# Kernel optimization log

Measured on AMD Instinct MI355X. Metric: run time of the kernel, lower is better.

## Reference

```python
import jax, jax.numpy as jnp
import numpy as np

N = 50000
EPS = 1e-5


def gcn_conv(x, edge_index, W, b):
    # x: [N, Fin] -> [N, Fout]; symmetric-normalized aggregation with self-loops
    h = x @ W  # [N, Fout]
    src = jnp.concatenate([edge_index[0], jnp.arange(N, dtype=edge_index.dtype)])
    dst = jnp.concatenate([edge_index[1], jnp.arange(N, dtype=edge_index.dtype)])
    deg = jax.ops.segment_sum(jnp.ones_like(dst, dtype=h.dtype), dst, num_segments=N)
    dinv = jnp.where(deg > 0, jax.lax.rsqrt(deg), 0.0)
    norm = dinv[src] * dinv[dst]  # [E+N]
    msg = h[src] * norm[:, None]  # [E+N, Fout]
    out = jax.ops.segment_sum(msg, dst, num_segments=N)
    return out + b


def batch_norm_eval(x, gamma, beta, mean, var):
    return (x - mean) * jax.lax.rsqrt(var + EPS) * gamma + beta


def setup_inputs() -> dict:
    key = jax.random.key(0)
    ks = jax.random.split(key, 16)
    Fin, H, C = 128, 64, 40
    inp = {
        "x": jax.random.normal(ks[0], (N, Fin), dtype=jnp.float32),
        "edge_index": jax.random.randint(ks[1], (2, 1600000), 0, N, dtype=jnp.int64),
        "W1": jax.random.normal(ks[2], (Fin, H), dtype=jnp.float32) / np.sqrt(Fin),
        "b1": jnp.zeros((H,), jnp.float32),
        "g1": jax.random.normal(ks[3], (H,), jnp.float32) * 0.1 + 1.0,
        "be1": jax.random.normal(ks[4], (H,), jnp.float32) * 0.1,
        "m1": jax.random.normal(ks[5], (H,), jnp.float32) * 0.1,
        "v1": jax.random.uniform(ks[6], (H,), jnp.float32, 0.5, 1.5),
        "W2": jax.random.normal(ks[7], (H, H), dtype=jnp.float32) / np.sqrt(H),
        "b2": jnp.zeros((H,), jnp.float32),
        "g2": jax.random.normal(ks[8], (H,), jnp.float32) * 0.1 + 1.0,
        "be2": jax.random.normal(ks[9], (H,), jnp.float32) * 0.1,
        "m2": jax.random.normal(ks[10], (H,), jnp.float32) * 0.1,
        "v2": jax.random.uniform(ks[11], (H,), jnp.float32, 0.5, 1.5),
        "W3": jax.random.normal(ks[12], (H, C), dtype=jnp.float32) / np.sqrt(H),
        "b3": jnp.zeros((C,), jnp.float32),
    }
    return inp


def reference(x, edge_index, W1, b1, g1, be1, m1, v1, W2, b2, g2, be2, m2, v2, W3, b3):
    # eval-mode forward: dropout is identity, BatchNorm uses running stats
    h = gcn_conv(x, edge_index, W1, b1)
    h = jax.nn.relu(batch_norm_eval(h, g1, be1, m1, v1))
    h = gcn_conv(h, edge_index, W2, b2)
    h = jax.nn.relu(batch_norm_eval(h, g2, be2, m2, v2))
    return gcn_conv(h, edge_index, W3, b3)
```

## Files before the change

kernel.cpp:

```cpp
#include <hip/hip_runtime.h>
#include <hip/hip_fp16.h>

#define BN_EPS 1e-5f

typedef _Float16 half2_t __attribute__((ext_vector_type(2)));
typedef _Float16 half8_t __attribute__((ext_vector_type(8)));

static __device__ __forceinline__ float fdot2(half2_t a, half2_t b, float c) {
    return __builtin_amdgcn_fdot2(a, b, c, false);
}


__global__ void k_zero(int* __restrict__ p, int n) {
    int i = threadIdx.x;
    if (i < n) p[i] = 0;
}

__global__ void k_bcount(const int* __restrict__ dst, int* __restrict__ btot, int E, int B) {
    __shared__ int cnt[256];
    int tid = threadIdx.x;
    cnt[tid] = 0;
    __syncthreads();
    int e0 = blockIdx.x * 2048;
#pragma unroll
    for (int j = 0; j < 8; ++j) {
        int e = e0 + j * 256 + tid;
        if (e < E) atomicAdd(&cnt[dst[e] >> 8], 1);
    }
    __syncthreads();
    if (tid < B && cnt[tid] > 0) atomicAdd(&btot[tid], cnt[tid]);
}

__global__ void k_bscan(const int* __restrict__ btot, int* __restrict__ bbase,
                        int* __restrict__ bcur, int* __restrict__ row_ptr, int N, int B) {
    __shared__ int sc[256];
    int tid = threadIdx.x;
    int v = (tid < B) ? btot[tid] : 0;
    sc[tid] = v;
    __syncthreads();
    for (int off = 1; off < 256; off <<= 1) {
        int t = (tid >= off) ? sc[tid - off] : 0;
        __syncthreads();
        sc[tid] += t;
        __syncthreads();
    }
    int excl = sc[tid] - v;
    if (tid < B) { bbase[tid] = excl; bcur[tid] = excl; }
    if (tid == B - 1) { bbase[B] = excl + v; row_ptr[N] = excl + v; }
}

__global__ void k_bscatter(const int* __restrict__ src, const int* __restrict__ dst,
                           int* bcur, unsigned int* __restrict__ ebuf, int E, int B) {
    __shared__ int cnt[256];
    __shared__ int gb[256];
    int tid = threadIdx.x;
    cnt[tid] = 0;
    __syncthreads();
    int e0 = blockIdx.x * 2048;
    int bk[8], rk[8];
    unsigned int pay[8];
#pragma unroll
    for (int j = 0; j < 8; ++j) {
        int e = e0 + j * 256 + tid;
        if (e < E) {
            int d = dst[e];
            int b = d >> 8;
            bk[j] = b;
            rk[j] = atomicAdd(&cnt[b], 1);
            pay[j] = (unsigned int)src[e] | ((unsigned int)(d & 255) << 16);
        } else {
            bk[j] = -1; rk[j] = 0; pay[j] = 0;
        }
    }
    __syncthreads();
    if (tid < B && cnt[tid] > 0) gb[tid] = atomicAdd(&bcur[tid], cnt[tid]);
    __syncthreads();
#pragma unroll
    for (int j = 0; j < 8; ++j)
        if (bk[j] >= 0) ebuf[gb[bk[j]] + rk[j]] = pay[j];
}

__global__ void k_bfinal(const unsigned int* __restrict__ ebuf, const int* __restrict__ bbase,
                         int* __restrict__ row_ptr, float* __restrict__ dinv,
                         unsigned short* __restrict__ col, int N) {
    __shared__ int cnt[256];
    __shared__ int sc[256];
    __shared__ int cur[256];
    int tid = threadIdx.x;
    int b = blockIdx.x;
    int node0 = b << 8;
    int ebeg = bbase[b], eend = bbase[b + 1];

    cnt[tid] = 0;
    __syncthreads();
    for (int i = ebeg + tid; i < eend; i += 256)
        atomicAdd(&cnt[ebuf[i] >> 16], 1);
    __syncthreads();
    int myc = cnt[tid];
    sc[tid] = myc;
    __syncthreads();
    for (int off = 1; off < 256; off <<= 1) {
        int t = (tid >= off) ? sc[tid - off] : 0;
        __syncthreads();
        sc[tid] += t;
        __syncthreads();
    }
    int excl = sc[tid] - myc;
    cur[tid] = ebeg + excl;
    int node = node0 + tid;
    if (node < N) {
        row_ptr[node] = ebeg + excl;
        dinv[node] = rsqrtf((float)(myc + 1));
    }
    __syncthreads();
    for (int i = ebeg + tid; i < eend; i += 256) {
        unsigned int p = ebuf[i];
        int dl = p >> 16;
        int pos = atomicAdd(&cur[dl], 1);
        col[pos] = (unsigned short)(p & 0xFFFFu);
    }
}

template <int K, int FOUT, bool FP16IN>
__launch_bounds__(256)
__global__ void k_gemm_scale(const void* __restrict__ Xv, const float* __restrict__ W,
                             const float* __restrict__ dinv, half2_t* __restrict__ HS, int N) {
    constexpr int KK = K / 2;
    constexpr int XSTR = (K == 128) ? 66 : 36;
    __shared__ half2_t xs2[64][XSTR];
    __shared__ half2_t wl2[KK][FOUT];
    int tid = threadIdx.x;
    int row0 = blockIdx.x * 64;

    if constexpr (FP16IN) {
        const _Float16* X = (const _Float16*)Xv;
        constexpr int U = 64 * K / 8;
        for (int u = tid; u < U; u += 256) {
            int row = u / (K / 8), q = u % (K / 8);
            int grow = row0 + row;
            uint4 v = make_uint4(0u, 0u, 0u, 0u);
            if (grow < N) v = *(const uint4*)&X[(size_t)grow * K + q * 8];
            *(uint4*)&xs2[row][q * 4] = v;
        }
    } else {
        const float* X = (const float*)Xv;
        constexpr int U = 64 * K / 4;
        for (int u = tid; u < U; u += 256) {
            int row = u / (K / 4), c = u % (K / 4);
            int grow = row0 + row;
            half2_t h0 = (half2_t)(_Float16)0, h1 = (half2_t)(_Float16)0;
            if (grow < N) {
                float4 v = *(const float4*)&X[(size_t)grow * K + c * 4];
                h0[0] = (_Float16)v.x; h0[1] = (_Float16)v.y;
                h1[0] = (_Float16)v.z; h1[1] = (_Float16)v.w;
            }
            xs2[row][2 * c] = h0;
            xs2[row][2 * c + 1] = h1;
        }
    }
    for (int i = tid; i < KK * FOUT; i += 256) {
        int kk = i / FOUT, f = i % FOUT;
        half2_t h;
        h[0] = (_Float16)W[(2 * kk) * FOUT + f];
        h[1] = (_Float16)W[(2 * kk + 1) * FOUT + f];
        wl2[kk][f] = h;
    }
    __syncthreads();

    int tc = tid & 15, tr = tid >> 4;
    if (4 * tc < FOUT) {
        float acc[4][4] = {};
#pragma unroll 4
        for (int kk = 0; kk < KK; ++kk) {
            half2_t a0 = xs2[4 * tr + 0][kk];
            half2_t a1 = xs2[4 * tr + 1][kk];
            half2_t a2 = xs2[4 * tr + 2][kk];
            half2_t a3 = xs2[4 * tr + 3][kk];
            half8_t wv = *(const half8_t*)&wl2[kk][4 * tc];
            half2_t w0 = {wv[0], wv[1]};
            half2_t w1 = {wv[2], wv[3]};
            half2_t w2 = {wv[4], wv[5]};
            half2_t w3 = {wv[6], wv[7]};
            acc[0][0] = fdot2(a0, w0, acc[0][0]); acc[0][1] = fdot2(a0, w1, acc[0][1]);
            acc[0][2] = fdot2(a0, w2, acc[0][2]); acc[0][3] = fdot2(a0, w3, acc[0][3]);
            acc[1][0] = fdot2(a1, w0, acc[1][0]); acc[1][1] = fdot2(a1, w1, acc[1][1]);
            acc[1][2] = fdot2(a1, w2, acc[1][2]); acc[1][3] = fdot2(a1, w3, acc[1][3]);
            acc[2][0] = fdot2(a2, w0, acc[2][0]); acc[2][1] = fdot2(a2, w1, acc[2][1]);
            acc[2][2] = fdot2(a2, w2, acc[2][2]); acc[2][3] = fdot2(a2, w3, acc[2][3]);
            acc[3][0] = fdot2(a3, w0, acc[3][0]); acc[3][1] = fdot2(a3, w1, acc[3][1]);
            acc[3][2] = fdot2(a3, w2, acc[3][2]); acc[3][3] = fdot2(a3, w3, acc[3][3]);
        }
#pragma unroll
        for (int i = 0; i < 4; ++i) {
            int row = row0 + 4 * tr + i;
            if (row < N) {
                float dv = dinv[row];
                half2_t p0, p1;
                p0[0] = (_Float16)(dv * acc[i][0]); p0[1] = (_Float16)(dv * acc[i][1]);
                p1[0] = (_Float16)(dv * acc[i][2]); p1[1] = (_Float16)(dv * acc[i][3]);
                HS[(size_t)row * (FOUT / 2) + 2 * tc] = p0;
                HS[(size_t)row * (FOUT / 2) + 2 * tc + 1] = p1;
            }
        }
    }
}

template <int FOUT, bool BN>
__launch_bounds__(256)
__global__ void k_agg(const half2_t* __restrict__ hs2, const unsigned short* __restrict__ col,
                      const int* __restrict__ row_ptr, const float* __restrict__ dinv,
                      const float* __restrict__ b, const float* __restrict__ g,
                      const float* __restrict__ be, const float* __restrict__ m,
                      const float* __restrict__ v, void* __restrict__ outv, int N) {
    constexpr int NP = FOUT / 2;
    int gtid = blockIdx.x * blockDim.x + threadIdx.x;
    int wave = gtid >> 6;
    int lane = gtid & 63;
    int half = lane >> 5;
    int l = lane & 31;
    int nwaves = (gridDim.x * blockDim.x) >> 6;
    bool active = l < NP;

    float b0 = 0.f, b1 = 0.f, s0f = 0.f, s1f = 0.f, t0f = 0.f, t1f = 0.f;
    if (active) {
        b0 = b[2 * l]; b1 = b[2 * l + 1];
        if (BN) {
            s0f = g[2 * l] * rsqrtf(v[2 * l] + BN_EPS);
            s1f = g[2 * l + 1] * rsqrtf(v[2 * l + 1] + BN_EPS);
            t0f = be[2 * l] - m[2 * l] * s0f;
            t1f = be[2 * l + 1] - m[2 * l + 1] * s1f;
        }
    }

    for (int node = wave; node < N; node += nwaves) {
        int beg = row_ptr[node], end = row_ptr[node + 1];
        float ax = 0.f, ay = 0.f, bx = 0.f, by = 0.f;
        float cx = 0.f, cy = 0.f, dx = 0.f, dy = 0.f;
        if (active && half == 0) {
            half2_t t = hs2[(size_t)node * NP + l];
            ax = (float)t[0]; ay = (float)t[1];
        }
        int e = beg + half;
        for (; e + 6 < end; e += 8) {
            int i0 = col[e], i1 = col[e + 2], i2 = col[e + 4], i3 = col[e + 6];
            if (active) {
                half2_t t0 = hs2[(size_t)i0 * NP + l];
                half2_t t1 = hs2[(size_t)i1 * NP + l];
                half2_t t2 = hs2[(size_t)i2 * NP + l];
                half2_t t3 = hs2[(size_t)i3 * NP + l];
                ax += (float)t0[0]; ay += (float)t0[1];
                bx += (float)t1[0]; by += (float)t1[1];
                cx += (float)t2[0]; cy += (float)t2[1];
                dx += (float)t3[0]; dy += (float)t3[1];
            }
        }
        for (; e < end; e += 2) {
            int i0 = col[e];
            if (active) {
                half2_t t0 = hs2[(size_t)i0 * NP + l];
                ax += (float)t0[0]; ay += (float)t0[1];
            }
        }
        float sx = (ax + bx) + (cx + dx);
        float sy = (ay + by) + (cy + dy);
        sx += __shfl_xor(sx, 32);
        sy += __shfl_xor(sy, 32);
        if (active && half == 0) {
            float dv = dinv[node];
            float o0 = dv * sx + b0;
            float o1 = dv * sy + b1;
            if (BN) {
                o0 = fmaxf(o0 * s0f + t0f, 0.0f);
                o1 = fmaxf(o1 * s1f + t1f, 0.0f);
                half2_t h;
                h[0] = (_Float16)o0; h[1] = (_Float16)o1;
                ((half2_t*)outv)[(size_t)node * NP + l] = h;
            } else {
                ((float2*)outv)[(size_t)node * NP + l] = make_float2(o0, o1);
            }
        }
    }
}


extern "C" void kernel_launch(void* const* d_in, const int* in_sizes, int n_in,
                              void* d_out, int out_size, void* d_ws, size_t ws_size,
                              hipStream_t stream) {
    const float* x   = (const float*)d_in[0];
    const int*   ei  = (const int*)d_in[1];
    const float* W1  = (const float*)d_in[2];
    const float* b1  = (const float*)d_in[3];
    const float* g1  = (const float*)d_in[4];
    const float* be1 = (const float*)d_in[5];
    const float* m1  = (const float*)d_in[6];
    const float* v1  = (const float*)d_in[7];
    const float* W2  = (const float*)d_in[8];
    const float* b2  = (const float*)d_in[9];
    const float* g2  = (const float*)d_in[10];
    const float* be2 = (const float*)d_in[11];
    const float* m2  = (const float*)d_in[12];
    const float* v2  = (const float*)d_in[13];
    const float* W3  = (const float*)d_in[14];
    const float* b3  = (const float*)d_in[15];

    const int FIN = 128, H = 64;
    int N = in_sizes[0] / FIN;
    int E = in_sizes[1] / 2;
    const int* src = ei;
    const int* dst = ei + E;
    int B = (N + 255) >> 8;

    char* ws = (char*)d_ws;
    size_t off = 0;
    auto carve = [&](size_t bytes) -> void* {
        void* p = ws + off;
        off += (bytes + 255) & ~(size_t)255;
        return p;
    };
    float*  dinv    = (float*)carve((size_t)N * 4);
    int*    row_ptr = (int*)carve((size_t)(N + 1) * 4);
    unsigned short* col = (unsigned short*)carve((size_t)E * 2);
    unsigned int*   ebuf = (unsigned int*)carve((size_t)E * 4);
    half2_t* hs     = (half2_t*)carve((size_t)N * H * 2);
    _Float16* y     = (_Float16*)carve((size_t)N * H * 2);
    int*    btot    = (int*)carve(512 * 4);
    int*    bbase   = (int*)carve(512 * 4);
    int*    bcur    = (int*)carve(512 * 4);
    (void)ws_size; (void)n_in; (void)out_size;

    int eb2k = (E + 2047) / 2048;

    k_zero<<<1, 256, 0, stream>>>(btot, B);
    k_bcount<<<eb2k, 256, 0, stream>>>(dst, btot, E, B);
    k_bscan<<<1, 256, 0, stream>>>(btot, bbase, bcur, row_ptr, N, B);
    k_bscatter<<<eb2k, 256, 0, stream>>>(src, dst, bcur, ebuf, E, B);
    k_bfinal<<<B, 256, 0, stream>>>(ebuf, bbase, row_ptr, dinv, col, N);

    int gb = (N + 63) / 64;
    k_gemm_scale<128, 64, false><<<gb, 256, 0, stream>>>(x, W1, dinv, hs, N);
    k_agg<64, true><<<4096, 256, 0, stream>>>(hs, col, row_ptr, dinv, b1, g1, be1, m1, v1, y, N);
    k_gemm_scale<64, 64, true><<<gb, 256, 0, stream>>>(y, W2, dinv, hs, N);
    k_agg<64, true><<<4096, 256, 0, stream>>>(hs, col, row_ptr, dinv, b2, g2, be2, m2, v2, y, N);
    k_gemm_scale<64, 40, true><<<gb, 256, 0, stream>>>(y, W3, dinv, hs, N);
    k_agg<40, false><<<4096, 256, 0, stream>>>(hs, col, row_ptr, dinv, b3, nullptr, nullptr, nullptr, nullptr,
                                               d_out, N);
}
```

Measured before the change: 234.0 us.

## Vectorize SpMM aggregation with 16-byte half8 loads and 8 edge groups per wave

Changes the aggregation kernel so each lane loads 8 fp16 features (16 bytes) instead of 2. A wave now processes 8 edges in parallel (8 lane groups of 8) instead of 2, and the groups are combined with a three-step xor-shuffle reduction. The goal is to cut memory instructions per gathered row and expose more edge-level parallelism per node. In exchange it needs more registers for 16 accumulators, adds shuffle work, and leaves lanes idle for FOUT=40 (5 of 8 lanes active) and for low-degree tails.

```diff
diff --git a/kernel.cpp b/kernel.cpp
--- a/kernel.cpp
+++ b/kernel.cpp
@@ -207,76 +207,86 @@
 
 template <int FOUT, bool BN>
 __launch_bounds__(256)
-__global__ void k_agg(const half2_t* __restrict__ hs2, const unsigned short* __restrict__ col,
+__global__ void k_agg(const half8_t* __restrict__ hs8, const unsigned short* __restrict__ col,
                       const int* __restrict__ row_ptr, const float* __restrict__ dinv,
                       const float* __restrict__ b, const float* __restrict__ g,
                       const float* __restrict__ be, const float* __restrict__ m,
                       const float* __restrict__ v, void* __restrict__ outv, int N) {
-    constexpr int NP = FOUT / 2;
+    constexpr int NS = FOUT / 8;
     int gtid = blockIdx.x * blockDim.x + threadIdx.x;
     int wave = gtid >> 6;
     int lane = gtid & 63;
-    int half = lane >> 5;
-    int l = lane & 31;
+    int g8 = lane >> 3;
+    int s = lane & 7;
     int nwaves = (gridDim.x * blockDim.x) >> 6;
-    bool active = l < NP;
-
-    float b0 = 0.f, b1 = 0.f, s0f = 0.f, s1f = 0.f, t0f = 0.f, t1f = 0.f;
-    if (active) {
-        b0 = b[2 * l]; b1 = b[2 * l + 1];
-        if (BN) {
-            s0f = g[2 * l] * rsqrtf(v[2 * l] + BN_EPS);
-            s1f = g[2 * l + 1] * rsqrtf(v[2 * l + 1] + BN_EPS);
-            t0f = be[2 * l] - m[2 * l] * s0f;
-            t1f = be[2 * l + 1] - m[2 * l + 1] * s1f;
+    bool act = s < NS;
+
+    float bias[8], sf[8], tf[8];
+    if (act) {
+#pragma unroll
+        for (int j = 0; j < 8; ++j) {
+            int f = 8 * s + j;
+            bias[j] = b[f];
+            if (BN) {
+                sf[j] = g[f] * rsqrtf(v[f] + BN_EPS);
+                tf[j] = be[f] - m[f] * sf[j];
+            }
         }
     }
 
     for (int node = wave; node < N; node += nwaves) {
         int beg = row_ptr[node], end = row_ptr[node + 1];
-        float ax = 0.f, ay = 0.f, bx = 0.f, by = 0.f;
-        float cx = 0.f, cy = 0.f, dx = 0.f, dy = 0.f;
-        if (active && half == 0) {
-            half2_t t = hs2[(size_t)node * NP + l];
-            ax = (float)t[0]; ay = (float)t[1];
-        }
-        int e = beg + half;
-        for (; e + 6 < end; e += 8) {
-            int i0 = col[e], i1 = col[e + 2], i2 = col[e + 4], i3 = col[e + 6];
-            if (active) {
-                half2_t t0 = hs2[(size_t)i0 * NP + l];
-                half2_t t1 = hs2[(size_t)i1 * NP + l];
-                half2_t t2 = hs2[(size_t)i2 * NP + l];
-                half2_t t3 = hs2[(size_t)i3 * NP + l];
-                ax += (float)t0[0]; ay += (float)t0[1];
-                bx += (float)t1[0]; by += (float)t1[1];
-                cx += (float)t2[0]; cy += (float)t2[1];
-                dx += (float)t3[0]; dy += (float)t3[1];
-            }
-        }
-        for (; e < end; e += 2) {
+        float acc0[8] = {}, acc1[8] = {};
+        if (act && g8 == 0) {
+            half8_t t = hs8[(size_t)node * NS + s];
+#pragma unroll
+            for (int j = 0; j < 8; ++j) acc0[j] = (float)t[j];
+        }
+        int e = beg + g8;
+        for (; e + 8 < end; e += 16) {
             int i0 = col[e];
-            if (active) {
-                half2_t t0 = hs2[(size_t)i0 * NP + l];
-                ax += (float)t0[0]; ay += (float)t0[1];
-            }
-        }
-        float sx = (ax + bx) + (cx + dx);
-        float sy = (ay + by) + (cy + dy);
-        sx += __shfl_xor(sx, 32);
-        sy += __shfl_xor(sy, 32);
-        if (active && half == 0) {
+            int i1 = col[e + 8];
+            if (act) {
+                half8_t t0 = hs8[(size_t)i0 * NS + s];
+                half8_t t1 = hs8[(size_t)i1 * NS + s];
+#pragma unroll
+                for (int j = 0; j < 8; ++j) { acc0[j] += (float)t0[j]; acc1[j] += (float)t1[j]; }
+            }
+        }
+        if (e < end) {
+            int i0 = col[e];
+            if (act) {
+                half8_t t0 = hs8[(size_t)i0 * NS + s];
+#pragma unroll
+                for (int j = 0; j < 8; ++j) acc0[j] += (float)t0[j];
+            }
+        }
+#pragma unroll
+        for (int j = 0; j < 8; ++j) {
+            float sj = acc0[j] + acc1[j];
+            sj += __shfl_xor(sj, 8);
+            sj += __shfl_xor(sj, 16);
+            sj += __shfl_xor(sj, 32);
+            acc0[j] = sj;
+        }
+        if (g8 == 0 && act) {
             float dv = dinv[node];
-            float o0 = dv * sx + b0;
-            float o1 = dv * sy + b1;
             if (BN) {
-                o0 = fmaxf(o0 * s0f + t0f, 0.0f);
-                o1 = fmaxf(o1 * s1f + t1f, 0.0f);
-                half2_t h;
-                h[0] = (_Float16)o0; h[1] = (_Float16)o1;
-                ((half2_t*)outv)[(size_t)node * NP + l] = h;
+                half8_t h;
+#pragma unroll
+                for (int j = 0; j < 8; ++j) {
+                    float o = dv * acc0[j] + bias[j];
+                    o = fmaxf(o * sf[j] + tf[j], 0.0f);
+                    h[j] = (_Float16)o;
+                }
+                ((half8_t*)outv)[(size_t)node * NS + s] = h;
             } else {
-                ((float2*)outv)[(size_t)node * NP + l] = make_float2(o0, o1);
+                float o[8];
+#pragma unroll
+                for (int j = 0; j < 8; ++j) o[j] = dv * acc0[j] + bias[j];
+                float* op = (float*)outv + (size_t)node * FOUT + 8 * s;
+                *(float4*)op = make_float4(o[0], o[1], o[2], o[3]);
+                *(float4*)(op + 4) = make_float4(o[4], o[5], o[6], o[7]);
             }
         }
     }
@@ -337,11 +347,12 @@
     k_bfinal<<<B, 256, 0, stream>>>(ebuf, bbase, row_ptr, dinv, col, N);
 
     int gb = (N + 63) / 64;
+    const half8_t* hs8 = (const half8_t*)hs;
     k_gemm_scale<128, 64, false><<<gb, 256, 0, stream>>>(x, W1, dinv, hs, N);
-    k_agg<64, true><<<4096, 256, 0, stream>>>(hs, col, row_ptr, dinv, b1, g1, be1, m1, v1, y, N);
+    k_agg<64, true><<<4096, 256, 0, stream>>>(hs8, col, row_ptr, dinv, b1, g1, be1, m1, v1, y, N);
     k_gemm_scale<64, 64, true><<<gb, 256, 0, stream>>>(y, W2, dinv, hs, N);
-    k_agg<64, true><<<4096, 256, 0, stream>>>(hs, col, row_ptr, dinv, b2, g2, be2, m2, v2, y, N);
+    k_agg<64, true><<<4096, 256, 0, stream>>>(hs8, col, row_ptr, dinv, b2, g2, be2, m2, v2, y, N);
     k_gemm_scale<64, 40, true><<<gb, 256, 0, stream>>>(y, W3, dinv, hs, N);
-    k_agg<40, false><<<4096, 256, 0, stream>>>(hs, col, row_ptr, dinv, b3, nullptr, nullptr, nullptr, nullptr,
+    k_agg<40, false><<<4096, 256, 0, stream>>>(hs8, col, row_ptr, dinv, b3, nullptr, nullptr, nullptr, nullptr,
                                                d_out, N);
 }
```

After: 220.9 us. 5.6% less time.
